# Kernel tuning notes

Measured on AMD Instinct MI355X. Metric: run time of the kernel, lower is better.

## Reference

```python
import jax, jax.numpy as jnp
import numpy as np

DIM = 256
NUM_HEADS = 8
HEAD_DIM = DIM // NUM_HEADS


def setup_inputs() -> dict:
    key = jax.random.key(0)
    k1, k2, k3, k4 = jax.random.split(key, 4)
    B, C, H, W = 16, DIM, 64, 64
    x = jax.random.normal(k1, (B, C, H, W), dtype=jnp.float32)
    # 1x1 convs as dense weight matrices [out_ch, in_ch]
    Wqkv = jax.random.normal(k2, (3 * DIM, DIM), dtype=jnp.float32) * (DIM ** -0.5)
    Wproj = jax.random.normal(k3, (DIM, DIM), dtype=jnp.float32) * (DIM ** -0.5)
    bproj = jax.random.normal(k4, (DIM,), dtype=jnp.float32) * 0.01
    return {"x": x, "Wqkv": Wqkv, "Wproj": Wproj, "bproj": bproj}


def reference(x, Wqkv, Wproj, bproj):
    B, C, H, W = x.shape
    N = H * W
    hd = C // NUM_HEADS

    # qkv: 1x1 conv (no bias) == channel matmul
    qkv = jnp.einsum('oc,bchw->bohw', Wqkv, x)  # [B, 3C, H, W]
    q, k, v = jnp.split(qkv, 3, axis=1)

    def to_heads(t):
        # b (h d) x y -> b h (x y) d
        return t.reshape(B, NUM_HEADS, hd, N).transpose(0, 1, 3, 2)

    q, k, v = to_heads(q), to_heads(k), to_heads(v)  # [B, h, N, d]

    # linear attention feature map + per-token normalization over d
    q = jax.nn.elu(q) + 1.0
    k = jax.nn.elu(k) + 1.0
    q = q / jnp.sum(q, axis=-1, keepdims=True)
    k = k / jnp.sum(k, axis=-1, keepdims=True)

    kv = jnp.einsum('bhnd,bhne->bhde', k, v)   # [B, h, d, d]
    out = jnp.einsum('bhnd,bhde->bhne', q, kv)  # [B, h, N, d]

    # b h (x y) d -> b (h d) x y
    out = out.transpose(0, 1, 3, 2).reshape(B, C, H, W)

    # proj: 1x1 conv with bias; drop_path is identity in eval mode
    out = jnp.einsum('oc,bchw->bohw', Wproj, out) + bproj[None, :, None, None]
    return out + x
```

## Files before the change

kernel.cpp:

```cpp
#include <hip/hip_runtime.h>
#include <stdint.h>
#include <stddef.h>

#define DIM   256
#define NH    8
#define HD    32
#define BATCH 16
#define NTOK  4096

typedef __attribute__((ext_vector_type(8))) short short8;
typedef __attribute__((ext_vector_type(4))) float f32x4;

__device__ __forceinline__ unsigned short f2bf(float x){
  unsigned u = __float_as_uint(x);
  u += 0x7fffu + ((u >> 16) & 1u);
  return (unsigned short)(u >> 16);
}
__device__ __forceinline__ float elu1(float v){
  return (v > 0.f) ? (v + 1.f) : __expf(v);
}
__device__ __forceinline__ void gload_lds16(const void* g, void* lds){
  __builtin_amdgcn_global_load_lds(
      (const __attribute__((address_space(1))) unsigned int*)g,
      (__attribute__((address_space(3))) unsigned int*)lds, 16, 0, 0);
}

__global__ __launch_bounds__(256) void k_transpose_x(const float* __restrict__ x,
                                                     unsigned short* __restrict__ xt){
  __shared__ float tile[64][65];
  const int b = blockIdx.z, c0 = blockIdx.y * 64, n0 = blockIdx.x * 64;
  const float* xb = x + (size_t)b * DIM * NTOK;
  const int t = threadIdx.x;
  #pragma unroll
  for (int p = 0; p < 4; p++){
    int idx = t + p * 256;
    int row = idx >> 4;
    int col = (idx & 15) << 2;
    float4 v = *(const float4*)(xb + (size_t)(c0 + row) * NTOK + n0 + col);
    tile[row][col] = v.x; tile[row][col+1] = v.y; tile[row][col+2] = v.z; tile[row][col+3] = v.w;
  }
  __syncthreads();
  unsigned short* xtb = xt + (size_t)b * NTOK * DIM;
  #pragma unroll
  for (int p = 0; p < 4; p++){
    int idx = t + p * 256;
    int nl = idx >> 4;
    int cl = (idx & 15) << 2;
    ushort4 o;
    o.x = f2bf(tile[cl+0][nl]); o.y = f2bf(tile[cl+1][nl]);
    o.z = f2bf(tile[cl+2][nl]); o.w = f2bf(tile[cl+3][nl]);
    *(ushort4*)(xtb + (size_t)(n0 + nl) * DIM + c0 + cl) = o;
  }
}

__global__ __launch_bounds__(256) void k_convert_w(const float* __restrict__ wqkv,
                                                   unsigned short* __restrict__ wq_bf){
  int i = blockIdx.x * 256 + threadIdx.x;
  int row = i >> 6;
  int c4 = (i & 63) * 4;
  int dst;
  if (row < 256)      dst = row;
  else if (row < 512){ int p = (row - 256) >> 6; int s = (row - 256) & 63; dst = 256 + p*128 + s; }
  else               { int p = (row - 512) >> 6; int s = (row - 512) & 63; dst = 256 + p*128 + 64 + s; }
  float4 v = *(const float4*)(wqkv + (size_t)row * DIM + c4);
  ushort4 o = { f2bf(v.x), f2bf(v.y), f2bf(v.z), f2bf(v.w) };
  *(ushort4*)(wq_bf + (size_t)dst * DIM + c4) = o;
}

__global__ __launch_bounds__(512, 1) void k_qkv8(const unsigned short* __restrict__ wbf,
                                                 const unsigned short* __restrict__ xt,
                                                 unsigned short* __restrict__ qn,
                                                 float* __restrict__ kvp){
  __shared__ __align__(16) unsigned short sh[33792];
  unsigned short* bsh = sh + 16384;
  const int t = threadIdx.x;
  const int w = t >> 6, l = t & 63;
  const int t16 = l & 15, quad = l >> 4;
  const int wm = w >> 1, wn = w & 1;
  const int bid = blockIdx.x;
  const int super = bid / 48;
  const int rem = bid - super * 48;
  const int m = rem >> 3, lx = rem & 7;
  const int chunk = super * 8 + lx;
  const int b = chunk >> 4, nt2 = chunk & 15;
  const int o0 = m * 128;
  const bool isQ = (o0 < 256);
  const unsigned short* Bb = xt + ((size_t)b * NTOK + (size_t)nt2 * 256) * DIM;
  const int rowL = (w*16 + t16) * DIM + quad*8;

  short8 a_reg[4][2][2];
  #pragma unroll
  for (int rp = 0; rp < 2; rp++){
    const unsigned short* srcA = wbf + (size_t)o0 * DIM + rowL + rp*128;
    gload_lds16(srcA,      sh +        (w*2+0)*512);
    gload_lds16(srcA + 32, sh +        (w*2+1)*512);
    gload_lds16(srcA + 64, sh + 8192 + (w*2+0)*512);
    gload_lds16(srcA + 96, sh + 8192 + (w*2+1)*512);
    asm volatile("s_waitcnt vmcnt(0)" ::: "memory");
    __builtin_amdgcn_s_barrier();
    #pragma unroll
    for (int cc = 0; cc < 2; cc++)
      #pragma unroll
      for (int i = 0; i < 2; i++)
        #pragma unroll
        for (int kk = 0; kk < 2; kk++)
          a_reg[rp*2+cc][i][kk] = *(const short8*)(sh + cc*8192 + ((wm*2+i)*2+kk)*512 + l*8);
    asm volatile("s_waitcnt lgkmcnt(0)" ::: "memory");
    __builtin_amdgcn_s_barrier();
  }

  gload_lds16(Bb + rowL,      sh +        (w*2+0)*512);
  gload_lds16(Bb + rowL + 32, sh +        (w*2+1)*512);
  gload_lds16(Bb + rowL + 64, sh + 8192 + (w*2+0)*512);
  gload_lds16(Bb + rowL + 96, sh + 8192 + (w*2+1)*512);

  f32x4 acc[2][4];
  #pragma unroll
  for (int i = 0; i < 2; i++)
    #pragma unroll
    for (int j = 0; j < 4; j++){ acc[i][j][0]=0.f; acc[i][j][1]=0.f; acc[i][j][2]=0.f; acc[i][j][3]=0.f; }
  f32x4 kvacc;
  kvacc[0]=0.f; kvacc[1]=0.f; kvacc[2]=0.f; kvacc[3]=0.f;

  #pragma unroll
  for (int s = 0; s < 8; s++){
    if (s < 7) { asm volatile("s_waitcnt vmcnt(2)" ::: "memory"); }
    else       { asm volatile("s_waitcnt vmcnt(0)" ::: "memory"); }
    __builtin_amdgcn_s_barrier();
    const unsigned short* bufc = sh + (s & 1) * 8192;
    #pragma unroll
    for (int kk = 0; kk < 2; kk++){
      short8 bb[4];
      #pragma unroll
      for (int j = 0; j < 4; j++) bb[j] = *(const short8*)(bufc + ((wn*4+j)*2+kk)*512 + l*8);
      #pragma unroll
      for (int i = 0; i < 2; i++)
        #pragma unroll
        for (int j = 0; j < 4; j++)
          acc[i][j] = __builtin_amdgcn_mfma_f32_16x16x32_bf16(a_reg[s&3][i][kk], bb[j], acc[i][j], 0, 0, 0);
    }
    __builtin_amdgcn_s_barrier();
    if (s < 6){
      const int s2 = s + 2;
      const unsigned short* src = Bb + (size_t)((s2 >> 2) * 128) * DIM + rowL + (s2 & 3) * 64;
      unsigned short* db = sh + (s & 1) * 8192;
      gload_lds16(src,      db + (w*2+0)*512);
      gload_lds16(src + 32, db + (w*2+1)*512);
    }
    if ((s & 3) == 3){
      const int n0 = (nt2*2 + (s >> 2)) * 128;
      if (isQ || wm < 2){
        #pragma unroll
        for (int i = 0; i < 2; i++)
          #pragma unroll
          for (int j = 0; j < 4; j++)
            #pragma unroll
            for (int r = 0; r < 4; r++) acc[i][j][r] = elu1(acc[i][j][r]);
        float sc[4];
        #pragma unroll
        for (int j = 0; j < 4; j++){
          float v = 0.f;
          #pragma unroll
          for (int i = 0; i < 2; i++)
            #pragma unroll
            for (int r = 0; r < 4; r++) v += acc[i][j][r];
          v += __shfl_xor(v, 16);
          v += __shfl_xor(v, 32);
          sc[j] = 1.0f / v;
        }
        #pragma unroll
        for (int i = 0; i < 2; i++)
          #pragma unroll
          for (int j = 0; j < 4; j++){
            float inv = sc[j];
            #pragma unroll
            for (int r = 0; r < 4; r++) acc[i][j][r] *= inv;
          }
      }
      if (isQ){
        #pragma unroll
        for (int i = 0; i < 2; i++)
          #pragma unroll
          for (int j = 0; j < 4; j++){
            int n_l = wn*64 + j*16 + t16;
            int o_l0 = wm*32 + i*16 + quad*4;
            ushort4 pk = { f2bf(acc[i][j][0]), f2bf(acc[i][j][1]),
                           f2bf(acc[i][j][2]), f2bf(acc[i][j][3]) };
            *(ushort4*)(bsh + n_l*136 + o_l0) = pk;
          }
        asm volatile("s_waitcnt lgkmcnt(0)" ::: "memory");
        __builtin_amdgcn_s_barrier();
        unsigned short* dst = qn + (size_t)b * NTOK * DIM;
        #pragma unroll
        for (int p2 = 0; p2 < 4; p2++){
          int gg = t + p2 * 512;
          int n_l = gg >> 4, c = gg & 15;
          uint4 v = *(const uint4*)(bsh + n_l*136 + c*8);
          *(uint4*)(dst + (size_t)(n0 + n_l) * DIM + o0 + c*8) = v;
        }
      } else {
        #pragma unroll
        for (int i = 0; i < 2; i++)
          #pragma unroll
          for (int j = 0; j < 4; j++){
            int n_l = wn*64 + j*16 + t16;
            #pragma unroll
            for (int r = 0; r < 4; r++){
              int o_l = wm*32 + i*16 + quad*4 + r;
              bsh[o_l*136 + n_l] = f2bf(acc[i][j][r]);
            }
          }
        asm volatile("s_waitcnt lgkmcnt(0)" ::: "memory");
        __builtin_amdgcn_s_barrier();
        const int hl = w >> 2, dh = (w >> 1) & 1, eh = w & 1;
        const unsigned short* kbase = bsh + (hl*32 + dh*16) * 136;
        const unsigned short* vbase = bsh + (64 + hl*32 + eh*16) * 136;
        #pragma unroll
        for (int kk2 = 0; kk2 < 4; kk2++){
          int nn = kk2*32 + quad*8;
          short8 afrag = *(const short8*)(kbase + t16*136 + nn);
          short8 bfrag = *(const short8*)(vbase + t16*136 + nn);
          kvacc = __builtin_amdgcn_mfma_f32_16x16x32_bf16(afrag, bfrag, kvacc, 0, 0, 0);
        }
      }
      if (s == 3){
        #pragma unroll
        for (int i = 0; i < 2; i++)
          #pragma unroll
          for (int j = 0; j < 4; j++){ acc[i][j][0]=0.f; acc[i][j][1]=0.f; acc[i][j][2]=0.f; acc[i][j][3]=0.f; }
      }
    }
  }

  if (!isQ){
    const int pp = (o0 >> 7) - 2;
    const int hl = w >> 2, dh = (w >> 1) & 1, eh = w & 1;
    float* dst = kvp + ((size_t)((b*8 + pp*2 + hl) * 16 + nt2)) * 1024;
    #pragma unroll
    for (int r = 0; r < 4; r++)
      dst[(dh*16 + quad*4 + r)*32 + eh*16 + t16] = kvacc[r];
  }
}

__global__ __launch_bounds__(256) void k_M(const float* __restrict__ kvp,
                                           const float* __restrict__ wproj,
                                           unsigned short* __restrict__ M){
  __shared__ float kvL[1024];
  __shared__ float wpL[8192];
  const int t = threadIdx.x;
  const int h = blockIdx.x, b = blockIdx.y;
  const float* pbase = kvp + (size_t)((b*8 + h) * 16) * 1024;
  {
    float4 a = {0.f,0.f,0.f,0.f};
    #pragma unroll
    for (int p = 0; p < 16; p++){
      float4 v = *(const float4*)(pbase + (size_t)p*1024 + t*4);
      a.x += v.x; a.y += v.y; a.z += v.z; a.w += v.w;
    }
    *(float4*)(kvL + t*4) = a;
  }
  #pragma unroll
  for (int p = 0; p < 8; p++){
    int idx = t + p * 256;
    int o = idx >> 3, e4 = idx & 7;
    *(float4*)(wpL + o*32 + e4*4) = *(const float4*)(wproj + (size_t)o * DIM + h*32 + e4*4);
  }
  __syncthreads();
  float wr[32];
  #pragma unroll
  for (int e = 0; e < 32; e++) wr[e] = wpL[t*32 + e];
  unsigned short md[32];
  #pragma unroll
  for (int d = 0; d < 32; d++){
    float a = 0.f;
    #pragma unroll
    for (int e = 0; e < 32; e++) a += wr[e] * kvL[d*32 + e];
    md[d] = f2bf(a);
  }
  unsigned short* dst = M + (size_t)b * 65536 + (size_t)t * DIM + h*32;
  #pragma unroll
  for (int q = 0; q < 4; q++) *(uint4*)(dst + q*8) = *(const uint4*)(md + q*8);
}

__global__ __launch_bounds__(512, 4) void k_out5(const unsigned short* __restrict__ M,
                                                 const unsigned short* __restrict__ qn,
                                                 const float* __restrict__ x,
                                                 const float* __restrict__ bproj,
                                                 float* __restrict__ out){
  __shared__ __align__(16) unsigned short As[8192];
  __shared__ __align__(16) unsigned short Bs[8192];
  const int t = threadIdx.x;
  const int w = t >> 6, l = t & 63;
  const int t16 = l & 15, quad = l >> 4;
  const int wm = w >> 1, wn = w & 1;
  const int bid = blockIdx.x;
  const int super = bid >> 4;
  const int rem = bid & 15;
  const int m = rem >> 3, lx = rem & 7;
  const int g = super * 8 + lx;
  const int nt = g >> 4, b = g & 15;
  const int o0 = m * 128, n0 = nt * 128;
  const unsigned short* A = qn + (size_t)b * NTOK * DIM;
  const unsigned short* Bm = M + (size_t)b * 65536;

  f32x4 acc[2][4];
  #pragma unroll
  for (int i = 0; i < 2; i++)
    #pragma unroll
    for (int j = 0; j < 4; j++){ acc[i][j][0]=0.f; acc[i][j][1]=0.f; acc[i][j][2]=0.f; acc[i][j][3]=0.f; }

  for (int k0 = 0; k0 < 256; k0 += 64){
    __syncthreads();
    #pragma unroll
    for (int s4 = 0; s4 < 4; s4++){
      int s = w * 4 + s4;
      int sl = s & 15;
      int tile = sl >> 1, kk = sl & 1;
      const unsigned short* src = (s < 16)
          ? (A  + (size_t)(n0 + tile*16 + t16) * DIM + k0 + kk*32 + quad*8)
          : (Bm + (size_t)(o0 + tile*16 + t16) * DIM + k0 + kk*32 + quad*8);
      gload_lds16(src, (s < 16) ? (As + sl * 512) : (Bs + sl * 512));
    }
    __syncthreads();
    #pragma unroll
    for (int kk = 0; kk < 2; kk++){
      short8 a[2], bb[4];
      #pragma unroll
      for (int i = 0; i < 2; i++) a[i]  = *(const short8*)(As + ((wm*2 + i)*2 + kk) * 512 + l * 8);
      #pragma unroll
      for (int j = 0; j < 4; j++) bb[j] = *(const short8*)(Bs + ((wn*4 + j)*2 + kk) * 512 + l * 8);
      #pragma unroll
      for (int i = 0; i < 2; i++)
        #pragma unroll
        for (int j = 0; j < 4; j++)
          acc[i][j] = __builtin_amdgcn_mfma_f32_16x16x32_bf16(a[i], bb[j], acc[i][j], 0, 0, 0);
    }
  }

  const float* xb = x + (size_t)b * DIM * NTOK;
  float* ob = out + (size_t)b * DIM * NTOK;
  #pragma unroll
  for (int j = 0; j < 4; j++){
    int o = o0 + wn*64 + j*16 + t16;
    float bias = bproj[o];
    #pragma unroll
    for (int i = 0; i < 2; i++){
      int n = n0 + wm*32 + i*16 + quad*4;
      float4 xv = *(const float4*)(xb + (size_t)o * NTOK + n);
      float4 res = { acc[i][j][0] + bias + xv.x,
                     acc[i][j][1] + bias + xv.y,
                     acc[i][j][2] + bias + xv.z,
                     acc[i][j][3] + bias + xv.w };
      *(float4*)(ob + (size_t)o * NTOK + n) = res;
    }
  }
}

extern "C" void kernel_launch(void* const* d_in, const int* in_sizes, int n_in,
                              void* d_out, int out_size, void* d_ws, size_t ws_size,
                              hipStream_t stream){
  const float* x     = (const float*)d_in[0];
  const float* wqkv  = (const float*)d_in[1];
  const float* wproj = (const float*)d_in[2];
  const float* bproj = (const float*)d_in[3];
  float* out = (float*)d_out;
  char* ws = (char*)d_ws;

  unsigned short* xt   = (unsigned short*)(ws);
  unsigned short* qn   = (unsigned short*)(ws + ((size_t)32 << 20));
  float* kvp           = (float*)(ws + ((size_t)64 << 20));
  unsigned short* M    = (unsigned short*)(ws + ((size_t)80 << 20));
  unsigned short* wqbf = (unsigned short*)(ws + ((size_t)82 << 20));

  k_transpose_x<<<dim3(64, 4, 16), 256, 0, stream>>>(x, xt);
  k_convert_w  <<<dim3(192), 256, 0, stream>>>(wqkv, wqbf);
  k_qkv8       <<<dim3(1536), 512, 0, stream>>>(wqbf, xt, qn, kvp);
  k_M          <<<dim3(8, 16), 256, 0, stream>>>(kvp, wproj, M);
  k_out5       <<<dim3(1024), 512, 0, stream>>>(M, qn, x, bproj, out);
}
```

Baseline: 224.7 us.

## Deepen qkv B-tile pipeline to four LDS buffers and defer first Q store

Measured after the change: 244.3 us. +8.8%, slower.

```diff
diff --git a/kernel.cpp b/kernel.cpp
--- a/kernel.cpp
+++ b/kernel.cpp
@@ -67,12 +67,12 @@
   *(ushort4*)(wq_bf + (size_t)dst * DIM + c4) = o;
 }
 
-__global__ __launch_bounds__(512, 1) void k_qkv8(const unsigned short* __restrict__ wbf,
+__global__ __launch_bounds__(512, 1) void k_qkv9(const unsigned short* __restrict__ wbf,
                                                  const unsigned short* __restrict__ xt,
                                                  unsigned short* __restrict__ qn,
                                                  float* __restrict__ kvp){
-  __shared__ __align__(16) unsigned short sh[33792];
-  unsigned short* bsh = sh + 16384;
+  __shared__ __align__(16) unsigned short sh[50176];
+  unsigned short* bsh = sh + 32768;
   const int t = threadIdx.x;
   const int w = t >> 6, l = t & 63;
   const int t16 = l & 15, quad = l >> 4;
@@ -86,33 +86,35 @@
   const int o0 = m * 128;
   const bool isQ = (o0 < 256);
   const unsigned short* Bb = xt + ((size_t)b * NTOK + (size_t)nt2 * 256) * DIM;
-  const int rowL = (w*16 + t16) * DIM + quad*8;
 
   short8 a_reg[4][2][2];
-  #pragma unroll
-  for (int rp = 0; rp < 2; rp++){
-    const unsigned short* srcA = wbf + (size_t)o0 * DIM + rowL + rp*128;
-    gload_lds16(srcA,      sh +        (w*2+0)*512);
-    gload_lds16(srcA + 32, sh +        (w*2+1)*512);
-    gload_lds16(srcA + 64, sh + 8192 + (w*2+0)*512);
-    gload_lds16(srcA + 96, sh + 8192 + (w*2+1)*512);
+  {
+    const unsigned short* srcA = wbf + (size_t)(o0 + w*16 + t16) * DIM + quad*8;
+    #pragma unroll
+    for (int c = 0; c < 4; c++){
+      gload_lds16(srcA + c*64,      sh + ((w*4 + c)*2 + 0)*512);
+      gload_lds16(srcA + c*64 + 32, sh + ((w*4 + c)*2 + 1)*512);
+    }
     asm volatile("s_waitcnt vmcnt(0)" ::: "memory");
     __builtin_amdgcn_s_barrier();
     #pragma unroll
-    for (int cc = 0; cc < 2; cc++)
+    for (int c = 0; c < 4; c++)
       #pragma unroll
       for (int i = 0; i < 2; i++)
         #pragma unroll
         for (int kk = 0; kk < 2; kk++)
-          a_reg[rp*2+cc][i][kk] = *(const short8*)(sh + cc*8192 + ((wm*2+i)*2+kk)*512 + l*8);
+          a_reg[c][i][kk] = *(const short8*)(sh + (((wm*2 + i)*4 + c)*2 + kk)*512 + l*8);
     asm volatile("s_waitcnt lgkmcnt(0)" ::: "memory");
     __builtin_amdgcn_s_barrier();
   }
 
-  gload_lds16(Bb + rowL,      sh +        (w*2+0)*512);
-  gload_lds16(Bb + rowL + 32, sh +        (w*2+1)*512);
-  gload_lds16(Bb + rowL + 64, sh + 8192 + (w*2+0)*512);
-  gload_lds16(Bb + rowL + 96, sh + 8192 + (w*2+1)*512);
+#define STAGE(ss) { \
+    const unsigned short* srcB = Bb + (size_t)((((ss) >> 2)*128) + w*16 + t16) * DIM + ((ss) & 3)*64 + quad*8; \
+    unsigned short* db = sh + ((ss) & 3) * 8192; \
+    gload_lds16(srcB,      db + (w*2 + 0)*512); \
+    gload_lds16(srcB + 32, db + (w*2 + 1)*512); }
+
+  STAGE(0); STAGE(1); STAGE(2);
 
   f32x4 acc[2][4];
   #pragma unroll
@@ -121,34 +123,29 @@
     for (int j = 0; j < 4; j++){ acc[i][j][0]=0.f; acc[i][j][1]=0.f; acc[i][j][2]=0.f; acc[i][j][3]=0.f; }
   f32x4 kvacc;
   kvacc[0]=0.f; kvacc[1]=0.f; kvacc[2]=0.f; kvacc[3]=0.f;
+  uint4 qsave[4];
 
   #pragma unroll
   for (int s = 0; s < 8; s++){
-    if (s < 7) { asm volatile("s_waitcnt vmcnt(2)" ::: "memory"); }
-    else       { asm volatile("s_waitcnt vmcnt(0)" ::: "memory"); }
+    if (s < 6)       { asm volatile("s_waitcnt vmcnt(4)" ::: "memory"); }
+    else if (s == 6) { asm volatile("s_waitcnt vmcnt(2)" ::: "memory"); }
+    else             { asm volatile("s_waitcnt vmcnt(0)" ::: "memory"); }
     __builtin_amdgcn_s_barrier();
-    const unsigned short* bufc = sh + (s & 1) * 8192;
+    const unsigned short* bufc = sh + (s & 3) * 8192;
     #pragma unroll
     for (int kk = 0; kk < 2; kk++){
       short8 bb[4];
       #pragma unroll
-      for (int j = 0; j < 4; j++) bb[j] = *(const short8*)(bufc + ((wn*4+j)*2+kk)*512 + l*8);
+      for (int j = 0; j < 4; j++) bb[j] = *(const short8*)(bufc + ((wn*4 + j)*2 + kk)*512 + l*8);
       #pragma unroll
       for (int i = 0; i < 2; i++)
         #pragma unroll
         for (int j = 0; j < 4; j++)
           acc[i][j] = __builtin_amdgcn_mfma_f32_16x16x32_bf16(a_reg[s&3][i][kk], bb[j], acc[i][j], 0, 0, 0);
     }
-    __builtin_amdgcn_s_barrier();
-    if (s < 6){
-      const int s2 = s + 2;
-      const unsigned short* src = Bb + (size_t)((s2 >> 2) * 128) * DIM + rowL + (s2 & 3) * 64;
-      unsigned short* db = sh + (s & 1) * 8192;
-      gload_lds16(src,      db + (w*2+0)*512);
-      gload_lds16(src + 32, db + (w*2+1)*512);
-    }
+    if (s < 5) STAGE(s + 3);
+
     if ((s & 3) == 3){
-      const int n0 = (nt2*2 + (s >> 2)) * 128;
       if (isQ || wm < 2){
         #pragma unroll
         for (int i = 0; i < 2; i++)
@@ -190,13 +187,24 @@
           }
         asm volatile("s_waitcnt lgkmcnt(0)" ::: "memory");
         __builtin_amdgcn_s_barrier();
-        unsigned short* dst = qn + (size_t)b * NTOK * DIM;
-        #pragma unroll
-        for (int p2 = 0; p2 < 4; p2++){
-          int gg = t + p2 * 512;
-          int n_l = gg >> 4, c = gg & 15;
-          uint4 v = *(const uint4*)(bsh + n_l*136 + c*8);
-          *(uint4*)(dst + (size_t)(n0 + n_l) * DIM + o0 + c*8) = v;
+        if (s == 3){
+          #pragma unroll
+          for (int p2 = 0; p2 < 4; p2++){
+            int gg = t + p2 * 512;
+            int n_l = gg >> 4, c = gg & 15;
+            qsave[p2] = *(const uint4*)(bsh + n_l*136 + c*8);
+          }
+          asm volatile("s_waitcnt lgkmcnt(0)" ::: "memory");
+        } else {
+          const int n0 = (nt2*2 + 1) * 128;
+          unsigned short* dst = qn + (size_t)b * NTOK * DIM;
+          #pragma unroll
+          for (int p2 = 0; p2 < 4; p2++){
+            int gg = t + p2 * 512;
+            int n_l = gg >> 4, c = gg & 15;
+            uint4 v = *(const uint4*)(bsh + n_l*136 + c*8);
+            *(uint4*)(dst + (size_t)(n0 + n_l) * DIM + o0 + c*8) = v;
+          }
         }
       } else {
         #pragma unroll
@@ -231,8 +239,18 @@
       }
     }
   }
-
-  if (!isQ){
+#undef STAGE
+
+  if (isQ){
+    const int n0 = (nt2*2) * 128;
+    unsigned short* dst = qn + (size_t)b * NTOK * DIM;
+    #pragma unroll
+    for (int p2 = 0; p2 < 4; p2++){
+      int gg = t + p2 * 512;
+      int n_l = gg >> 4, c = gg & 15;
+      *(uint4*)(dst + (size_t)(n0 + n_l) * DIM + o0 + c*8) = qsave[p2];
+    }
+  } else {
     const int pp = (o0 >> 7) - 2;
     const int hl = w >> 2, dh = (w >> 1) & 1, eh = w & 1;
     float* dst = kvp + ((size_t)((b*8 + pp*2 + hl) * 16 + nt2)) * 1024;
@@ -374,7 +392,7 @@
 
   k_transpose_x<<<dim3(64, 4, 16), 256, 0, stream>>>(x, xt);
   k_convert_w  <<<dim3(192), 256, 0, stream>>>(wqkv, wqbf);
-  k_qkv8       <<<dim3(1536), 512, 0, stream>>>(wqbf, xt, qn, kvp);
+  k_qkv9       <<<dim3(1536), 512, 0, stream>>>(wqbf, xt, qn, kvp);
   k_M          <<<dim3(8, 16), 256, 0, stream>>>(kvp, wproj, M);
   k_out5       <<<dim3(1024), 512, 0, stream>>>(M, qn, x, bproj, out);
 }
```
